# Optimization experiments

Hardware: AMD Instinct MI355X
Metric: run time of the kernel (lower is better)

Reference implementation:

```python
import jax, jax.numpy as jnp
import numpy as np

N_USERS = 100000
N_ITEMS = 200000
N_NODES = N_USERS + N_ITEMS
EMB_DIM = 64
N_EDGES = 4000000
N_LAYERS = 2
BATCH = 8192
EMB_REG = 2.5e-5


def setup_inputs() -> dict:
    key = jax.random.key(0)
    k = jax.random.split(key, 7)
    return {
        "user_emb": jax.random.normal(k[0], (N_USERS, EMB_DIM), jnp.float32) * 0.1,
        "item_emb": jax.random.normal(k[1], (N_ITEMS, EMB_DIM), jnp.float32) * 0.1,
        "all_h": jax.random.randint(k[2], (N_EDGES,), 0, N_NODES, jnp.int64 if jax.config.jax_enable_x64 else jnp.int32),
        "all_t": jax.random.randint(k[3], (N_EDGES,), 0, N_NODES, jnp.int64 if jax.config.jax_enable_x64 else jnp.int32),
        "users": jax.random.randint(k[4], (BATCH,), 0, N_USERS),
        "pos_items": jax.random.randint(k[5], (BATCH,), 0, N_ITEMS),
        "neg_items": jax.random.randint(k[6], (BATCH,), 0, N_ITEMS),
    }


def _spmm(h, t, vals, x):
    # out[h] += vals * x[t]  over all edges; [N_NODES, D]
    return jax.ops.segment_sum(vals[:, None] * x[t], h, num_segments=N_NODES)


def reference(user_emb, item_emb, all_h, all_t, users, pos_items, neg_items):
    # symmetric normalization G = D^{-1/2} A D^{-1/2} on the edge list
    deg = jax.ops.segment_sum(jnp.ones((all_h.shape[0],), user_emb.dtype), all_h,
                              num_segments=N_NODES)
    dinv = jnp.where(deg > 0, deg ** -0.5, 0.0)
    g_vals = dinv[all_h] * dinv[all_t]

    # inference1: n_layers of SpMM with residual; sum over all layer outputs
    # (dropout p=0 on the main branch in the source -> identity)
    emb = jnp.concatenate([user_emb, item_emb], axis=0)  # [N, D]
    acc = emb
    for _ in range(N_LAYERS):
        emb = _spmm(all_h, all_t, g_vals, emb) + emb
        acc = acc + emb
    ua, ia = acc[:N_USERS], acc[N_USERS:]

    # BPR loss on the batch
    u = ua[users]
    pos = ia[pos_items]
    neg = ia[neg_items]
    pos_scores = jnp.sum(u * pos, axis=1)
    neg_scores = jnp.sum(u * neg, axis=1)
    mf_loss = jnp.mean(jax.nn.softplus(neg_scores - pos_scores))

    # embedding L2 regularization on the pre-propagation embeddings
    u_pre = user_emb[users]
    pos_pre = item_emb[pos_items]
    neg_pre = item_emb[neg_items]
    emb_loss = EMB_REG * (jnp.sum(u_pre ** 2) + jnp.sum(pos_pre ** 2)
                          + jnp.sum(neg_pre ** 2))
    return (mf_loss, emb_loss)
```

## Files before the change

kernel.cpp:

```cpp
#include <hip/hip_runtime.h>
#include <math.h>

#define N_USERS 100000
#define N_ITEMS 200000
#define N_NODES 300000
#define EMB_DIM 64
#define N_EDGES 4000000
#define BATCH   8192
#define EMB_REG 2.5e-05f

#define BUCK_SH 9
#define BN      512
#define NBUCK   586
#define BSLOT   7424
#define EPB     8192
#define EPT     32
#define NBLK_A  489
#define NBLK_MARK (BATCH / 256)
#define PACK_SH 19
#define SCORE_BLOCKS (BATCH / 4)

typedef unsigned short u16;
typedef unsigned int   u32;
typedef unsigned char  u8;
typedef __attribute__((ext_vector_type(8))) u16 u16x8;
typedef __attribute__((ext_vector_type(2))) float f32x2;

__device__ __forceinline__ float bf2f(u16 x) {
    u32 u = ((u32)x) << 16;
    return __builtin_bit_cast(float, u);
}
__device__ __forceinline__ u16 f2bf(float f) {
    u32 u = __builtin_bit_cast(u32, f);
    return (u16)((u + 0x7FFFu + ((u >> 16) & 1u)) >> 16);
}

__global__ __launch_bounds__(256) void kA(const int* __restrict__ hh,
                                          const int* __restrict__ tt,
                                          int* __restrict__ bcur, int* __restrict__ gp,
                                          const int* __restrict__ users,
                                          const int* __restrict__ pos,
                                          const int* __restrict__ neg,
                                          u8* __restrict__ flags,
                                          u8* __restrict__ e0s8) {
    if (blockIdx.x >= NBLK_A) {
        int i = (blockIdx.x - NBLK_A) * 256 + threadIdx.x;
        if (i < BATCH) {
            flags[users[i]] = 1;
            flags[N_USERS + pos[i]] = 1;
            flags[N_USERS + neg[i]] = 1;
        }
        if (blockIdx.x == NBLK_A && threadIdx.x < 16)
            ((int*)(e0s8 + (size_t)N_NODES * EMB_DIM))[threadIdx.x] = 0;
        return;
    }
    __shared__ int sh_cnt[NBUCK];
    __shared__ int sh_off[NBUCK];
    __shared__ int sh_base[NBUCK];
    __shared__ int stage[EPB];
    __shared__ u16 sbid[EPB];
    int tid = threadIdx.x;
    for (int j = tid; j < NBUCK; j += 256) sh_cnt[j] = 0;
    __syncthreads();
    int cbase = blockIdx.x * EPB;
    int clen  = min(EPB, N_EDGES - cbase);
    int pk[EPT], bk[EPT];
    #pragma unroll
    for (int j = 0; j < EPT; ++j) {
        int i = j * 256 + tid;
        bk[j] = -1;
        if (i < clen) {
            int h = hh[cbase + i];
            int t = tt[cbase + i];
            int b = h >> BUCK_SH;
            bk[j] = b;
            pk[j] = ((h & (BN - 1)) << PACK_SH) | t;
            atomicAdd(&sh_cnt[b], 1);
        }
    }
    __syncthreads();
    if (tid < 64) {
        int lane = tid, carry = 0;
        for (int b0 = 0; b0 < NBUCK; b0 += 64) {
            int idx = b0 + lane;
            int v = (idx < NBUCK) ? sh_cnt[idx] : 0;
            int incl = v;
            #pragma unroll
            for (int d = 1; d < 64; d <<= 1) {
                int u = __shfl_up(incl, d, 64);
                if (lane >= d) incl += u;
            }
            if (idx < NBUCK) sh_off[idx] = carry + incl - v;
            carry += __shfl(incl, 63, 64);
        }
    }
    __syncthreads();
    for (int j = tid; j < NBUCK; j += 256) {
        int c = sh_cnt[j];
        sh_base[j] = j * BSLOT + (c ? atomicAdd(&bcur[j], c) : 0);
        sh_cnt[j] = 0;
    }
    __syncthreads();
    #pragma unroll
    for (int j = 0; j < EPT; ++j) {
        if (bk[j] >= 0) {
            int r = atomicAdd(&sh_cnt[bk[j]], 1);
            int p = sh_off[bk[j]] + r;
            stage[p] = pk[j];
            sbid[p]  = (u16)bk[j];
        }
    }
    __syncthreads();
    for (int i = tid; i < clen; i += 256) {
        int b = sbid[i];
        gp[sh_base[b] + i - sh_off[b]] = stage[i];
    }
}

__global__ __launch_bounds__(256) void kB(const int* __restrict__ bcur,
                                          int* __restrict__ gp,
                                          int2* __restrict__ sde, float* __restrict__ dinv,
                                          const float* __restrict__ uemb,
                                          const float* __restrict__ iemb,
                                          u8* __restrict__ e0s8) {
    __shared__ int   ncnt[BN];
    __shared__ int   noff[BN];
    __shared__ float sdv[BN];
    __shared__ int   slots[BSLOT];
    int b = blockIdx.x;
    int node0 = b << BUCK_SH;
    int nn = min(BN, N_NODES - node0);
    int base = b * BSLOT;
    int count = bcur[b];
    int tid = threadIdx.x;
    for (int j = tid; j < BN; j += 256) ncnt[j] = 0;
    __syncthreads();
    for (int i = tid; i < count; i += 256)
        atomicAdd(&ncnt[gp[base + i] >> PACK_SH], 1);
    __syncthreads();
    if (tid < 64) {
        int lane = tid, carry = 0;
        #pragma unroll
        for (int b0 = 0; b0 < BN; b0 += 64) {
            int idx = b0 + lane;
            int v = ncnt[idx];
            int incl = v;
            #pragma unroll
            for (int d = 1; d < 64; d <<= 1) {
                int u = __shfl_up(incl, d, 64);
                if (lane >= d) incl += u;
            }
            noff[idx] = carry + incl - v;
            carry += __shfl(incl, 63, 64);
        }
    }
    __syncthreads();
    for (int j = tid; j < nn; j += 256) {
        int c = ncnt[j];
        float dv = c > 0 ? rsqrtf((float)c) : 0.0f;
        sde[node0 + j]  = make_int2(base + noff[j], c);
        dinv[node0 + j] = dv;
        sdv[j] = dv;
    }
    __syncthreads();
    for (int j = tid; j < BN; j += 256) ncnt[j] = noff[j];
    __syncthreads();
    for (int i = tid; i < count; i += 256) {
        int p = gp[base + i];
        int r = atomicAdd(&ncnt[p >> PACK_SH], 1);
        slots[r] = p & ((1 << PACK_SH) - 1);
    }
    __syncthreads();
    for (int i = tid; i < count; i += 256)
        gp[base + i] = slots[i];
    for (int i = tid; i < nn * 8; i += 256) {
        int j = i >> 3;
        float sc = sdv[j];
        int gnode = node0 + j;
        size_t ebase = (size_t)gnode * EMB_DIM + (size_t)(i & 7) * 8;
        const size_t UELEMS = (size_t)N_USERS * EMB_DIM;
        const float* src = (ebase < UELEMS) ? uemb + ebase : iemb + (ebase - UELEMS);
        float4 a  = ((const float4*)src)[0];
        float4 c4 = ((const float4*)src)[1];
        u32 w0 = __builtin_amdgcn_cvt_pk_fp8_f32(sc * a.x,  sc * a.y,  0,  false);
        w0 = __builtin_amdgcn_cvt_pk_fp8_f32(sc * a.z,  sc * a.w,  w0, true);
        u32 w1 = __builtin_amdgcn_cvt_pk_fp8_f32(sc * c4.x, sc * c4.y, 0,  false);
        w1 = __builtin_amdgcn_cvt_pk_fp8_f32(sc * c4.z, sc * c4.w, w1, true);
        uint2 o; o.x = w0; o.y = w1;
        ((uint2*)e0s8)[(size_t)gnode * 8 + (i & 7)] = o;
    }
}

__global__ __launch_bounds__(256) void k_spmm1(const int2* __restrict__ sde,
                        const int* __restrict__ et,
                        const u8* __restrict__ src8,
                        const float* __restrict__ uemb, const float* __restrict__ iemb,
                        const u8* __restrict__ flags,
                        u16* __restrict__ dstb, u8* __restrict__ dst8) {
    int lane = threadIdx.x & 63;
    int g    = lane >> 2;
    int sl   = lane & 3;
    int gb   = lane & 60;
    int node = blockIdx.x * 64 + ((threadIdx.x >> 6) << 4) + g;
    bool alive = node < N_NODES;
    int2 se = alive ? sde[node] : make_int2(0, 0);
    int s = se.x, ne = se.y;
    float dh = ne > 0 ? rsqrtf((float)ne) : 0.0f;
    float acc[16];
    #pragma unroll
    for (int k = 0; k < 16; ++k) acc[k] = 0.f;
    int nb = (ne + 3) & ~3;
    for (int j0 = 0; j0 < nb; j0 += 4) {
        int idx = j0 + sl;
        int ets = (idx < ne) ? et[s + idx] : N_NODES;
        #pragma unroll
        for (int jj = 0; jj < 4; ++jj) {
            int t = __shfl(ets, gb | jj, 64);
            uint4 d8 = ((const uint4*)(src8 + (size_t)t * EMB_DIM))[sl];
            f32x2 p;
            p = __builtin_amdgcn_cvt_pk_f32_fp8(d8.x, false); acc[0]  += p.x; acc[1]  += p.y;
            p = __builtin_amdgcn_cvt_pk_f32_fp8(d8.x, true);  acc[2]  += p.x; acc[3]  += p.y;
            p = __builtin_amdgcn_cvt_pk_f32_fp8(d8.y, false); acc[4]  += p.x; acc[5]  += p.y;
            p = __builtin_amdgcn_cvt_pk_f32_fp8(d8.y, true);  acc[6]  += p.x; acc[7]  += p.y;
            p = __builtin_amdgcn_cvt_pk_f32_fp8(d8.z, false); acc[8]  += p.x; acc[9]  += p.y;
            p = __builtin_amdgcn_cvt_pk_f32_fp8(d8.z, true);  acc[10] += p.x; acc[11] += p.y;
            p = __builtin_amdgcn_cvt_pk_f32_fp8(d8.w, false); acc[12] += p.x; acc[13] += p.y;
            p = __builtin_amdgcn_cvt_pk_f32_fp8(d8.w, true);  acc[14] += p.x; acc[15] += p.y;
        }
    }
    if (!alive) {
        if (node == N_NODES) {
            uint4 z; z.x = 0; z.y = 0; z.z = 0; z.w = 0;
            ((uint4*)(dst8 + (size_t)N_NODES * EMB_DIM))[sl] = z;
        }
        return;
    }
    const float* srow = (node < N_USERS)
        ? uemb + (size_t)node * EMB_DIM
        : iemb + (size_t)(node - N_USERS) * EMB_DIM;
    float4 a0 = ((const float4*)srow)[sl * 4 + 0];
    float4 a1 = ((const float4*)srow)[sl * 4 + 1];
    float4 a2 = ((const float4*)srow)[sl * 4 + 2];
    float4 a3 = ((const float4*)srow)[sl * 4 + 3];
    float v[16];
    v[0]  = dh * acc[0]  + a0.x; v[1]  = dh * acc[1]  + a0.y;
    v[2]  = dh * acc[2]  + a0.z; v[3]  = dh * acc[3]  + a0.w;
    v[4]  = dh * acc[4]  + a1.x; v[5]  = dh * acc[5]  + a1.y;
    v[6]  = dh * acc[6]  + a1.z; v[7]  = dh * acc[7]  + a1.w;
    v[8]  = dh * acc[8]  + a2.x; v[9]  = dh * acc[9]  + a2.y;
    v[10] = dh * acc[10] + a2.z; v[11] = dh * acc[11] + a2.w;
    v[12] = dh * acc[12] + a3.x; v[13] = dh * acc[13] + a3.y;
    v[14] = dh * acc[14] + a3.z; v[15] = dh * acc[15] + a3.w;
    uint4 ow;
    u32 w;
    w = __builtin_amdgcn_cvt_pk_fp8_f32(dh * v[0],  dh * v[1],  0, false);
    w = __builtin_amdgcn_cvt_pk_fp8_f32(dh * v[2],  dh * v[3],  w, true);  ow.x = w;
    w = __builtin_amdgcn_cvt_pk_fp8_f32(dh * v[4],  dh * v[5],  0, false);
    w = __builtin_amdgcn_cvt_pk_fp8_f32(dh * v[6],  dh * v[7],  w, true);  ow.y = w;
    w = __builtin_amdgcn_cvt_pk_fp8_f32(dh * v[8],  dh * v[9],  0, false);
    w = __builtin_amdgcn_cvt_pk_fp8_f32(dh * v[10], dh * v[11], w, true);  ow.z = w;
    w = __builtin_amdgcn_cvt_pk_fp8_f32(dh * v[12], dh * v[13], 0, false);
    w = __builtin_amdgcn_cvt_pk_fp8_f32(dh * v[14], dh * v[15], w, true);  ow.w = w;
    ((uint4*)(dst8 + (size_t)node * EMB_DIM))[sl] = ow;
    if (flags[node]) {
        u16x8 o0, o1;
        o0.s0 = f2bf(v[0]);  o0.s1 = f2bf(v[1]);  o0.s2 = f2bf(v[2]);  o0.s3 = f2bf(v[3]);
        o0.s4 = f2bf(v[4]);  o0.s5 = f2bf(v[5]);  o0.s6 = f2bf(v[6]);  o0.s7 = f2bf(v[7]);
        o1.s0 = f2bf(v[8]);  o1.s1 = f2bf(v[9]);  o1.s2 = f2bf(v[10]); o1.s3 = f2bf(v[11]);
        o1.s4 = f2bf(v[12]); o1.s5 = f2bf(v[13]); o1.s6 = f2bf(v[14]); o1.s7 = f2bf(v[15]);
        ((u16x8*)(dstb + (size_t)node * EMB_DIM))[sl * 2]     = o0;
        ((u16x8*)(dstb + (size_t)node * EMB_DIM))[sl * 2 + 1] = o1;
    }
}

__global__ void k_score(const int* __restrict__ users, const int* __restrict__ pos,
                        const int* __restrict__ neg,
                        const float* __restrict__ uemb, const float* __restrict__ iemb,
                        const u16* __restrict__ emb1b, const u8* __restrict__ emb1s8,
                        const int2* __restrict__ sde, const int* __restrict__ et,
                        const float* __restrict__ dinv,
                        float* __restrict__ pmf, float* __restrict__ psq) {
    __shared__ float smf[4], ssq[4];
    int gid = blockIdx.x * blockDim.x + threadIdx.x;
    int b = gid >> 6;
    int d = gid & 63;
    int w = threadIdx.x >> 6;
    int u  = users[b];
    int pi = pos[b];
    int ni = neg[b];
    int nodes[3];
    nodes[0] = u; nodes[1] = N_USERS + pi; nodes[2] = N_USERS + ni;
    float pre[3];
    pre[0] = uemb[(size_t)u * EMB_DIM + d];
    pre[1] = iemb[(size_t)pi * EMB_DIM + d];
    pre[2] = iemb[(size_t)ni * EMB_DIM + d];
    int s0[3], ne[3], ets[3], lim[3];
    float dv[3];
    #pragma unroll
    for (int k = 0; k < 3; ++k) {
        int v = nodes[k];
        int2 se = sde[v];
        s0[k] = se.x; ne[k] = se.y;
        dv[k] = dinv[v];
        ets[k] = (d < ne[k]) ? et[se.x + d] : 0;
        lim[k] = ne[k] < 64 ? ne[k] : 64;
    }
    int lmax = max(lim[0], max(lim[1], lim[2]));
    float ac[3] = {0.f, 0.f, 0.f};
    for (int j = 0; j < lmax; j += 2) {
        u32 by[6];
        #pragma unroll
        for (int k = 0; k < 3; ++k) {
            int t0 = (j     < lim[k]) ? __shfl(ets[k], j,     64) : N_NODES;
            int t1 = (j + 1 < lim[k]) ? __shfl(ets[k], j + 1, 64) : N_NODES;
            by[k * 2]     = emb1s8[(size_t)t0 * EMB_DIM + d];
            by[k * 2 + 1] = emb1s8[(size_t)t1 * EMB_DIM + d];
        }
        #pragma unroll
        for (int k = 0; k < 3; ++k) {
            ac[k] += __builtin_amdgcn_cvt_f32_fp8(by[k * 2],     0);
            ac[k] += __builtin_amdgcn_cvt_f32_fp8(by[k * 2 + 1], 0);
        }
    }
    float a[3];
    #pragma unroll
    for (int k = 0; k < 3; ++k) {
        float acx = ac[k];
        for (int i = s0[k] + 64; i < s0[k] + ne[k]; ++i) {
            int t = et[i];
            u32 byte = emb1s8[(size_t)t * EMB_DIM + d];
            acx += __builtin_amdgcn_cvt_f32_fp8(byte, 0);
        }
        a[k] = pre[k] + 2.0f * bf2f(emb1b[(size_t)nodes[k] * EMB_DIM + d]) + dv[k] * acx;
    }
    float ps = a[0] * a[1];
    float ns = a[0] * a[2];
    float sq = pre[0] * pre[0] + pre[1] * pre[1] + pre[2] * pre[2];
    #pragma unroll
    for (int off2 = 32; off2 > 0; off2 >>= 1) {
        ps += __shfl_down(ps, off2, 64);
        ns += __shfl_down(ns, off2, 64);
        sq += __shfl_down(sq, off2, 64);
    }
    if (d == 0) {
        float x  = ns - ps;
        smf[w] = fmaxf(x, 0.0f) + log1pf(expf(-fabsf(x)));
        ssq[w] = sq;
    }
    __syncthreads();
    if (threadIdx.x == 0) {
        pmf[blockIdx.x] = smf[0] + smf[1] + smf[2] + smf[3];
        psq[blockIdx.x] = ssq[0] + ssq[1] + ssq[2] + ssq[3];
    }
}

__global__ void k_final(const float* __restrict__ pmf, const float* __restrict__ psq,
                        float* __restrict__ out) {
    __shared__ float smf[4], ssq[4];
    int tid = threadIdx.x;
    float mf = 0.f, sq = 0.f;
    #pragma unroll
    for (int i = 0; i < SCORE_BLOCKS / 256; ++i) {
        mf += pmf[tid + i * 256];
        sq += psq[tid + i * 256];
    }
    #pragma unroll
    for (int off2 = 32; off2 > 0; off2 >>= 1) {
        mf += __shfl_down(mf, off2, 64);
        sq += __shfl_down(sq, off2, 64);
    }
    if ((tid & 63) == 0) { smf[tid >> 6] = mf; ssq[tid >> 6] = sq; }
    __syncthreads();
    if (tid == 0) {
        out[0] = (smf[0] + smf[1] + smf[2] + smf[3]) * (1.0f / BATCH);
        out[1] = EMB_REG * (ssq[0] + ssq[1] + ssq[2] + ssq[3]);
    }
}

extern "C" void kernel_launch(void* const* d_in, const int* in_sizes, int n_in,
                              void* d_out, int out_size, void* d_ws, size_t ws_size,
                              hipStream_t stream) {
    const float* uemb  = (const float*)d_in[0];
    const float* iemb  = (const float*)d_in[1];
    const int*   all_h = (const int*)d_in[2];
    const int*   all_t = (const int*)d_in[3];
    const int*   users = (const int*)d_in[4];
    const int*   pos   = (const int*)d_in[5];
    const int*   neg   = (const int*)d_in[6];
    float* out = (float*)d_out;

    int*   ws     = (int*)d_ws;
    float* dinv   = (float*)ws;
    int2*  sde    = (int2*)(ws + 300032);
    u8*    flags  = (u8*)(ws + 900096);
    int*   bcur   = ws + 975104;
    float* pmf    = (float*)(ws + 976128);
    float* psq    = (float*)(ws + 978176);
    int*   gp     = ws + 980224;
    u8*    e0s8   = (u8*)(ws + 5330688);
    u8*    emb1s8 = (u8*)(ws + 10130944);
    u16*   emb1b  = (u16*)(ws + 14930960);

    hipMemsetAsync(flags, 0, 304128, stream);

    kA <<<NBLK_A + NBLK_MARK, 256, 0, stream>>>(all_h, all_t, bcur, gp,
                                                users, pos, neg, flags, e0s8);
    kB <<<NBUCK, 256, 0, stream>>>(bcur, gp, sde, dinv, uemb, iemb, e0s8);

    k_spmm1<<<(N_NODES + 63) / 64, 256, 0, stream>>>(sde, gp, e0s8, uemb, iemb,
                                                     flags, emb1b, emb1s8);

    k_score<<<SCORE_BLOCKS, 256, 0, stream>>>(users, pos, neg, uemb, iemb,
                                              emb1b, emb1s8, sde, gp, dinv, pmf, psq);
    k_final<<<1, 256, 0, stream>>>(pmf, psq, out);
}
```

Before: 284.3 us.

## Restructure score kernel so 4-lane groups gather whole fp8 rows per node

After: 284.3 us. Within noise of the previous version (-0.0%).

```diff
diff --git a/kernel.cpp b/kernel.cpp
--- a/kernel.cpp
+++ b/kernel.cpp
@@ -18,7 +18,7 @@
 #define NBLK_A  489
 #define NBLK_MARK (BATCH / 256)
 #define PACK_SH 19
-#define SCORE_BLOCKS (BATCH / 4)
+#define SCORE2_BLOCKS (BATCH / 16)
 
 typedef unsigned short u16;
 typedef unsigned int   u32;
@@ -273,82 +273,97 @@
     }
 }
 
-__global__ void k_score(const int* __restrict__ users, const int* __restrict__ pos,
-                        const int* __restrict__ neg,
-                        const float* __restrict__ uemb, const float* __restrict__ iemb,
-                        const u16* __restrict__ emb1b, const u8* __restrict__ emb1s8,
-                        const int2* __restrict__ sde, const int* __restrict__ et,
-                        const float* __restrict__ dinv,
-                        float* __restrict__ pmf, float* __restrict__ psq) {
+__global__ __launch_bounds__(256) void k_score2(
+        const int* __restrict__ users, const int* __restrict__ pos,
+        const int* __restrict__ neg,
+        const float* __restrict__ uemb, const float* __restrict__ iemb,
+        const u16* __restrict__ emb1b, const u8* __restrict__ emb1s8,
+        const int2* __restrict__ sde, const int* __restrict__ et,
+        const float* __restrict__ dinv,
+        float* __restrict__ pmf, float* __restrict__ psq) {
+    __shared__ float accL[3 * 16 * 64];
     __shared__ float smf[4], ssq[4];
-    int gid = blockIdx.x * blockDim.x + threadIdx.x;
-    int b = gid >> 6;
-    int d = gid & 63;
-    int w = threadIdx.x >> 6;
-    int u  = users[b];
-    int pi = pos[b];
-    int ni = neg[b];
-    int nodes[3];
-    nodes[0] = u; nodes[1] = N_USERS + pi; nodes[2] = N_USERS + ni;
-    float pre[3];
-    pre[0] = uemb[(size_t)u * EMB_DIM + d];
-    pre[1] = iemb[(size_t)pi * EMB_DIM + d];
-    pre[2] = iemb[(size_t)ni * EMB_DIM + d];
-    int s0[3], ne[3], ets[3], lim[3];
-    float dv[3];
-    #pragma unroll
-    for (int k = 0; k < 3; ++k) {
-        int v = nodes[k];
-        int2 se = sde[v];
-        s0[k] = se.x; ne[k] = se.y;
-        dv[k] = dinv[v];
-        ets[k] = (d < ne[k]) ? et[se.x + d] : 0;
-        lim[k] = ne[k] < 64 ? ne[k] : 64;
-    }
-    int lmax = max(lim[0], max(lim[1], lim[2]));
-    float ac[3] = {0.f, 0.f, 0.f};
-    for (int j = 0; j < lmax; j += 2) {
-        u32 by[6];
+    int tid  = threadIdx.x;
+    int wv   = tid >> 6;
+    int lane = tid & 63;
+    int g    = lane >> 2;
+    int sl   = lane & 3;
+    int gb   = lane & 60;
+    int B0   = blockIdx.x * 16;
+
+    if (wv < 3) {
+        int b = B0 + g;
+        int node = (wv == 0) ? users[b]
+                 : (wv == 1) ? (N_USERS + pos[b])
+                             : (N_USERS + neg[b]);
+        int2 se = sde[node];
+        int s = se.x, ne = se.y;
+        float acc[16];
         #pragma unroll
-        for (int k = 0; k < 3; ++k) {
-            int t0 = (j     < lim[k]) ? __shfl(ets[k], j,     64) : N_NODES;
-            int t1 = (j + 1 < lim[k]) ? __shfl(ets[k], j + 1, 64) : N_NODES;
-            by[k * 2]     = emb1s8[(size_t)t0 * EMB_DIM + d];
-            by[k * 2 + 1] = emb1s8[(size_t)t1 * EMB_DIM + d];
-        }
+        for (int i = 0; i < 16; ++i) acc[i] = 0.f;
+        int nb = (ne + 3) & ~3;
+        for (int j0 = 0; j0 < nb; j0 += 4) {
+            int idx = j0 + sl;
+            int ets = (idx < ne) ? et[s + idx] : N_NODES;
+            #pragma unroll
+            for (int jj = 0; jj < 4; ++jj) {
+                int t = __shfl(ets, gb | jj, 64);
+                uint4 d8 = ((const uint4*)(emb1s8 + (size_t)t * EMB_DIM))[sl];
+                f32x2 p;
+                p = __builtin_amdgcn_cvt_pk_f32_fp8(d8.x, false); acc[0]  += p.x; acc[1]  += p.y;
+                p = __builtin_amdgcn_cvt_pk_f32_fp8(d8.x, true);  acc[2]  += p.x; acc[3]  += p.y;
+                p = __builtin_amdgcn_cvt_pk_f32_fp8(d8.y, false); acc[4]  += p.x; acc[5]  += p.y;
+                p = __builtin_amdgcn_cvt_pk_f32_fp8(d8.y, true);  acc[6]  += p.x; acc[7]  += p.y;
+                p = __builtin_amdgcn_cvt_pk_f32_fp8(d8.z, false); acc[8]  += p.x; acc[9]  += p.y;
+                p = __builtin_amdgcn_cvt_pk_f32_fp8(d8.z, true);  acc[10] += p.x; acc[11] += p.y;
+                p = __builtin_amdgcn_cvt_pk_f32_fp8(d8.w, false); acc[12] += p.x; acc[13] += p.y;
+                p = __builtin_amdgcn_cvt_pk_f32_fp8(d8.w, true);  acc[14] += p.x; acc[15] += p.y;
+            }
+        }
+        float* dst = &accL[((wv * 16 + g) << 6) + (sl << 4)];
+        ((float4*)dst)[0] = make_float4(acc[0],  acc[1],  acc[2],  acc[3]);
+        ((float4*)dst)[1] = make_float4(acc[4],  acc[5],  acc[6],  acc[7]);
+        ((float4*)dst)[2] = make_float4(acc[8],  acc[9],  acc[10], acc[11]);
+        ((float4*)dst)[3] = make_float4(acc[12], acc[13], acc[14], acc[15]);
+    }
+    __syncthreads();
+    float mfl = 0.f, sql = 0.f;
+    int d = lane;
+    #pragma unroll
+    for (int q = 0; q < 4; ++q) {
+        int bl = wv * 4 + q;
+        int b  = B0 + bl;
+        int u  = users[b];
+        int pi = pos[b];
+        int ni = neg[b];
+        int n0 = u, n1 = N_USERS + pi, n2 = N_USERS + ni;
+        float pre0 = uemb[(size_t)u  * EMB_DIM + d];
+        float pre1 = iemb[(size_t)pi * EMB_DIM + d];
+        float pre2 = iemb[(size_t)ni * EMB_DIM + d];
+        float a0 = pre0 + 2.0f * bf2f(emb1b[(size_t)n0 * EMB_DIM + d])
+                 + dinv[n0] * accL[((0 * 16 + bl) << 6) + d];
+        float a1 = pre1 + 2.0f * bf2f(emb1b[(size_t)n1 * EMB_DIM + d])
+                 + dinv[n1] * accL[((1 * 16 + bl) << 6) + d];
+        float a2 = pre2 + 2.0f * bf2f(emb1b[(size_t)n2 * EMB_DIM + d])
+                 + dinv[n2] * accL[((2 * 16 + bl) << 6) + d];
+        float ps = a0 * a1;
+        float ns = a0 * a2;
+        float sq = pre0 * pre0 + pre1 * pre1 + pre2 * pre2;
         #pragma unroll
-        for (int k = 0; k < 3; ++k) {
-            ac[k] += __builtin_amdgcn_cvt_f32_fp8(by[k * 2],     0);
-            ac[k] += __builtin_amdgcn_cvt_f32_fp8(by[k * 2 + 1], 0);
-        }
-    }
-    float a[3];
-    #pragma unroll
-    for (int k = 0; k < 3; ++k) {
-        float acx = ac[k];
-        for (int i = s0[k] + 64; i < s0[k] + ne[k]; ++i) {
-            int t = et[i];
-            u32 byte = emb1s8[(size_t)t * EMB_DIM + d];
-            acx += __builtin_amdgcn_cvt_f32_fp8(byte, 0);
-        }
-        a[k] = pre[k] + 2.0f * bf2f(emb1b[(size_t)nodes[k] * EMB_DIM + d]) + dv[k] * acx;
-    }
-    float ps = a[0] * a[1];
-    float ns = a[0] * a[2];
-    float sq = pre[0] * pre[0] + pre[1] * pre[1] + pre[2] * pre[2];
-    #pragma unroll
-    for (int off2 = 32; off2 > 0; off2 >>= 1) {
-        ps += __shfl_down(ps, off2, 64);
-        ns += __shfl_down(ns, off2, 64);
-        sq += __shfl_down(sq, off2, 64);
-    }
-    if (d == 0) {
-        float x  = ns - ps;
-        smf[w] = fmaxf(x, 0.0f) + log1pf(expf(-fabsf(x)));
-        ssq[w] = sq;
-    }
-    __syncthreads();
-    if (threadIdx.x == 0) {
+        for (int off2 = 32; off2 > 0; off2 >>= 1) {
+            ps += __shfl_down(ps, off2, 64);
+            ns += __shfl_down(ns, off2, 64);
+            sq += __shfl_down(sq, off2, 64);
+        }
+        if (lane == 0) {
+            float x = ns - ps;
+            mfl += fmaxf(x, 0.0f) + log1pf(expf(-fabsf(x)));
+            sql += sq;
+        }
+    }
+    if (lane == 0) { smf[wv] = mfl; ssq[wv] = sql; }
+    __syncthreads();
+    if (tid == 0) {
         pmf[blockIdx.x] = smf[0] + smf[1] + smf[2] + smf[3];
         psq[blockIdx.x] = ssq[0] + ssq[1] + ssq[2] + ssq[3];
     }
@@ -360,7 +375,7 @@
     int tid = threadIdx.x;
     float mf = 0.f, sq = 0.f;
     #pragma unroll
-    for (int i = 0; i < SCORE_BLOCKS / 256; ++i) {
+    for (int i = 0; i < SCORE2_BLOCKS / 256; ++i) {
         mf += pmf[tid + i * 256];
         sq += psq[tid + i * 256];
     }
@@ -410,7 +425,8 @@
     k_spmm1<<<(N_NODES + 63) / 64, 256, 0, stream>>>(sde, gp, e0s8, uemb, iemb,
                                                      flags, emb1b, emb1s8);
 
-    k_score<<<SCORE_BLOCKS, 256, 0, stream>>>(users, pos, neg, uemb, iemb,
-                                              emb1b, emb1s8, sde, gp, dinv, pmf, psq);
+    k_score2<<<SCORE2_BLOCKS, 256, 0, stream>>>(users, pos, neg, uemb, iemb,
+                                                emb1b, emb1s8, sde, gp, dinv,
+                                                pmf, psq);
     k_final<<<1, 256, 0, stream>>>(pmf, psq, out);
 }
```
